# Optimization experiments

Hardware: AMD Instinct MI355X
Metric: run time of the kernel (lower is better)

The kernel has to match this reference:

```python
import jax, jax.numpy as jnp
import numpy as np

N, V, E, C_IN, C_OUT = 4, 4096, 2048, 64, 64


def setup_inputs() -> dict:
    key = jax.random.key(0)
    k_x, k_h, k_th = jax.random.split(key, 3)
    x = jax.random.normal(k_x, (N, V, C_IN), dtype=jnp.float32)
    H = (jax.random.uniform(k_h, (N, V, E)) < 0.05).astype(jnp.float32)
    # guarantee every vertex and every hyperedge has degree >= 1 (code divides by degree)
    v_idx = jnp.arange(V)
    H = H.at[:, v_idx, v_idx % E].set(1.0)
    # xavier_uniform for theta
    limit = float(np.sqrt(6.0 / (C_IN + C_OUT)))
    theta = jax.random.uniform(k_th, (C_IN, C_OUT), minval=-limit, maxval=limit, dtype=jnp.float32)
    bias = jnp.zeros((C_OUT,), dtype=jnp.float32)
    return {"x": x, "H": H, "theta": theta, "bias": bias}


def reference(x, H, theta, bias):
    # x: [N,V,C], H: [N,V,E] incidence, theta: [C,O], bias: [O]
    # Original builds diag_embed(1/deg) and multiplies; equivalent to direct
    # per-row / per-column scaling of H (same math, no NxVxV / NxExE diagonals).
    dv = 1.0 / H.sum(-1)            # [N,V] vertex degrees
    de = 1.0 / H.sum(1)             # [N,E] hyperedge degrees
    y = jnp.einsum('nvc,co->nvo', x, theta)          # [N,V,O]
    HDe = H * de[:, None, :]                          # H @ De  -> [N,V,E]
    y = jnp.einsum('nvc,nve->nec', y, HDe)            # vertex -> edge  [N,E,O]
    HDv = H * dv[:, :, None]                          # Dv @ H -> [N,V,E]
    y = jnp.einsum('nec,nve->nvc', y, HDv)            # edge -> vertex  [N,V,O]
    return y + bias[None, None, :]
```

## Files before the change

### kernel.cpp

```cpp
#include <hip/hip_runtime.h>
#include <hip/hip_bf16.h>
#include <stdint.h>

#define N_B 4
#define NV 4096
#define NE 2048
#define NC 64

typedef float    f32x4  __attribute__((ext_vector_type(4)));
typedef __bf16   bf16x8 __attribute__((ext_vector_type(8)));
typedef unsigned short u16;
typedef u16      u16x8  __attribute__((ext_vector_type(8)));
typedef uint32_t u32x4  __attribute__((ext_vector_type(4)));

__device__ __forceinline__ u16 f2bf_rne(float f) {
    uint32_t u = __builtin_bit_cast(uint32_t, f);
    u += 0x7FFFu + ((u >> 16) & 1u);
    return (u16)(u >> 16);
}
__device__ __forceinline__ float bf2f(u16 h) {
    uint32_t u = ((uint32_t)h) << 16;
    return __builtin_bit_cast(float, u);
}
__device__ __forceinline__ f32x4 mfma_bf16(u16x8 a, u16x8 b, f32x4 c) {
    return __builtin_amdgcn_mfma_f32_16x16x32_bf16(
        __builtin_bit_cast(bf16x8, a), __builtin_bit_cast(bf16x8, b), c, 0, 0, 0);
}
__device__ __forceinline__ u16x8 expand8(uint32_t byte) {
    u32x4 w;
#pragma unroll
    for (int p = 0; p < 4; ++p) {
        const uint32_t lo = (byte >> (2 * p)) & 1u;
        const uint32_t hi = (byte >> (2 * p + 1)) & 1u;
        w[p] = (lo | (hi << 16)) * 0x3F80u;
    }
    return __builtin_bit_cast(u16x8, w);
}

__global__ __launch_bounds__(256) void k_pack(const float* __restrict__ H,
                                              uint32_t* __restrict__ HB,
                                              uint32_t* __restrict__ HT,
                                              float* __restrict__ dvP,
                                              float* __restrict__ deP) {
    __shared__ float tile[64][65];
    const int n  = blockIdx.z;
    const int v0 = blockIdx.y * 64;
    const int e0 = blockIdx.x * 64;
    const int t = threadIdx.x, w = t >> 6, l = t & 63;

    const float* __restrict__ Hn = H + ((size_t)n * NV + v0) * NE + e0;

#pragma unroll 4
    for (int i = 0; i < 16; ++i) {
        const int row = w * 16 + i;
        const float h = Hn[(size_t)row * NE + l];
        tile[row][l] = h;
        const unsigned long long m = __ballot(h != 0.0f);
        if (l == 0)
            dvP[((size_t)blockIdx.x * N_B + n) * NV + v0 + row] = (float)__popcll(m);
        if (l < 2)
            HB[(((size_t)n * (NV / 16) + ((v0 + row) >> 4)) * (NE / 32) + (e0 >> 5) + l) * 16 +
               ((v0 + row) & 15)] = (uint32_t)(m >> (32 * l));
    }
    __syncthreads();

#pragma unroll 4
    for (int i = 0; i < 16; ++i) {
        const int col = w * 16 + i;
        const float h = tile[l][col];
        const unsigned long long m = __ballot(h != 0.0f);
        if (l == 0)
            deP[((size_t)blockIdx.y * N_B + n) * NE + e0 + col] = (float)__popcll(m);
        if (l < 2)
            HT[(((size_t)n * (NE / 16) + ((e0 + col) >> 4)) * (NV / 32) + (v0 >> 5) + l) * 16 +
               ((e0 + col) & 15)] = (uint32_t)(m >> (32 * l));
    }
}

__global__ __launch_bounds__(256) void k_deg(const float* __restrict__ dvP,
                                             const float* __restrict__ deP,
                                             float* __restrict__ dv,
                                             float* __restrict__ de) {
    const int id = blockIdx.x * 256 + threadIdx.x;
    if (id < N_B * NE) {
        float s = 0.f;
        for (int vt = 0; vt < 64; ++vt) s += deP[(size_t)vt * (N_B * NE) + id];
        de[id] = s;
    } else {
        const int j = id - N_B * NE;
        float s = 0.f;
        for (int et = 0; et < 32; ++et) s += dvP[(size_t)et * (N_B * NV) + j];
        dv[j] = s;
    }
}

__global__ __launch_bounds__(256) void k_xtheta(const float* __restrict__ x,
                                                const float* __restrict__ th,
                                                u16* __restrict__ Yh,
                                                u16* __restrict__ Yl) {
    __shared__ float xs[64][65];
    __shared__ float ts[64][65];
    const int t = threadIdx.x;
    const int n  = blockIdx.x >> 6;
    const int v0 = (blockIdx.x & 63) * 64;

#pragma unroll
    for (int i = 0; i < 4; ++i) {
        const int idx = i * 256 + t;
        const int row = idx >> 4, q = (idx & 15) * 4;
        const float4 xv = *(const float4*)&x[((size_t)(n * NV + v0 + row)) * 64 + q];
        const float4 tv = *(const float4*)&th[(size_t)row * 64 + q];
        xs[row][q] = xv.x; xs[row][q + 1] = xv.y; xs[row][q + 2] = xv.z; xs[row][q + 3] = xv.w;
        ts[row][q] = tv.x; ts[row][q + 1] = tv.y; ts[row][q + 2] = tv.z; ts[row][q + 3] = tv.w;
    }
    __syncthreads();

    const int v4 = (t & 15) * 4;
    const int c4 = (t >> 4) * 4;
    float acc[4][4] = {};
#pragma unroll
    for (int k = 0; k < 64; ++k) {
        float tv[4], xv[4];
#pragma unroll
        for (int i = 0; i < 4; ++i) { tv[i] = ts[k][c4 + i]; xv[i] = xs[v4 + i][k]; }
#pragma unroll
        for (int i = 0; i < 4; ++i)
#pragma unroll
            for (int j = 0; j < 4; ++j) acc[i][j] += tv[i] * xv[j];
    }
#pragma unroll
    for (int i = 0; i < 4; ++i) {
        ushort4 hi, lo;
        u16 h;
        h = f2bf_rne(acc[i][0]); hi.x = h; lo.x = f2bf_rne(acc[i][0] - bf2f(h));
        h = f2bf_rne(acc[i][1]); hi.y = h; lo.y = f2bf_rne(acc[i][1] - bf2f(h));
        h = f2bf_rne(acc[i][2]); hi.z = h; lo.z = f2bf_rne(acc[i][2] - bf2f(h));
        h = f2bf_rne(acc[i][3]); hi.w = h; lo.w = f2bf_rne(acc[i][3] - bf2f(h));
        const size_t o = ((size_t)n * 64 + c4 + i) * NV + v0 + v4;
        *(ushort4*)&Yh[o] = hi;
        *(ushort4*)&Yl[o] = lo;
    }
}

__global__ __launch_bounds__(256) void k_v2e(const uint32_t* __restrict__ HT,
                                             const u16* __restrict__ Yh,
                                             const u16* __restrict__ Yl,
                                             float* __restrict__ P2) {
    const int n  = blockIdx.z;
    const int sp = blockIdx.y;
    const int e0 = blockIdx.x * 64;
    const int krange = NV / gridDim.y;
    const int kk0 = sp * krange;
    const int S   = krange / 32;

    const int t = threadIdx.x, w = t >> 6, l = t & 63;
    const int lq = l >> 4, lr = l & 15;
    const int sh = lq * 8;

    const uint32_t* __restrict__ ht =
        HT + ((size_t)n * (NE / 16) + (e0 >> 4)) * ((NV / 32) * 16) + (kk0 >> 5) * 16 + lr;
    const u16* __restrict__ ybh = Yh + ((size_t)n * 64 + w * 16 + lr) * NV + kk0 + lq * 8;
    const u16* __restrict__ ybl = Yl + ((size_t)n * 64 + w * 16 + lr) * NV + kk0 + lq * 8;

    f32x4 acc0 = {0.f,0.f,0.f,0.f}, acc1 = acc0, acc2 = acc0, acc3 = acc0;

#pragma unroll 2
    for (int s = 0; s < S; ++s) {
        const u16x8 bh = *(const u16x8*)(ybh + s * 32);
        const u16x8 bl = *(const u16x8*)(ybl + s * 32);
        const uint32_t w0 = ht[0 * ((NV / 32) * 16) + s * 16];
        const uint32_t w1 = ht[1 * ((NV / 32) * 16) + s * 16];
        const uint32_t w2 = ht[2 * ((NV / 32) * 16) + s * 16];
        const uint32_t w3 = ht[3 * ((NV / 32) * 16) + s * 16];
        u16x8 a;
        a = expand8((w0 >> sh) & 0xFF);
        acc0 = mfma_bf16(a, bh, acc0); acc0 = mfma_bf16(a, bl, acc0);
        a = expand8((w1 >> sh) & 0xFF);
        acc1 = mfma_bf16(a, bh, acc1); acc1 = mfma_bf16(a, bl, acc1);
        a = expand8((w2 >> sh) & 0xFF);
        acc2 = mfma_bf16(a, bh, acc2); acc2 = mfma_bf16(a, bl, acc2);
        a = expand8((w3 >> sh) & 0xFF);
        acc3 = mfma_bf16(a, bh, acc3); acc3 = mfma_bf16(a, bl, acc3);
    }

    float* pb = P2 + (((size_t)sp * N_B + n) * 64 + w * 16 + lr) * NE + e0 + lq * 4;
    *(f32x4*)(pb + 0)  = acc0;
    *(f32x4*)(pb + 16) = acc1;
    *(f32x4*)(pb + 32) = acc2;
    *(f32x4*)(pb + 48) = acc3;
}

__global__ __launch_bounds__(256) void k_red2(const float* __restrict__ P2,
                                              const float* __restrict__ de,
                                              u16* __restrict__ Zh,
                                              u16* __restrict__ Zl, int nsp) {
    const int i = blockIdx.x * 256 + threadIdx.x;
    const int row = i >> 9;
    const int e4  = (i & 511) * 4;
    const int n   = row >> 6;

    float4 a = make_float4(0.f, 0.f, 0.f, 0.f);
    for (int sp = 0; sp < nsp; ++sp) {
        const float4 p = *(const float4*)&P2[((size_t)sp * 256 + row) * NE + e4];
        a.x += p.x; a.y += p.y; a.z += p.z; a.w += p.w;
    }
    const float4 d = *(const float4*)&de[(size_t)n * NE + e4];
    float z[4] = {a.x / d.x, a.y / d.y, a.z / d.z, a.w / d.w};
    ushort4 hi, lo;
    u16 h;
    h = f2bf_rne(z[0]); hi.x = h; lo.x = f2bf_rne(z[0] - bf2f(h));
    h = f2bf_rne(z[1]); hi.y = h; lo.y = f2bf_rne(z[1] - bf2f(h));
    h = f2bf_rne(z[2]); hi.z = h; lo.z = f2bf_rne(z[2] - bf2f(h));
    h = f2bf_rne(z[3]); hi.w = h; lo.w = f2bf_rne(z[3] - bf2f(h));
    *(ushort4*)&Zh[(size_t)row * NE + e4] = hi;
    *(ushort4*)&Zl[(size_t)row * NE + e4] = lo;
}

__global__ __launch_bounds__(256) void k_e2v(const uint32_t* __restrict__ HB,
                                             const u16* __restrict__ Zh,
                                             const u16* __restrict__ Zl,
                                             float* __restrict__ P3) {
    const int n  = blockIdx.z;
    const int sp = blockIdx.y;
    const int v0 = blockIdx.x * 64;
    const int krange = NE / gridDim.y;
    const int kk0 = sp * krange;
    const int S   = krange / 32;

    const int t = threadIdx.x, w = t >> 6, l = t & 63;
    const int lq = l >> 4, lr = l & 15;
    const int sh = lq * 8;

    const uint32_t* __restrict__ hb =
        HB + ((size_t)n * (NV / 16) + (v0 >> 4)) * ((NE / 32) * 16) + (kk0 >> 5) * 16 + lr;
    const u16* __restrict__ zbh = Zh + ((size_t)n * 64 + w * 16 + lr) * NE + kk0 + lq * 8;
    const u16* __restrict__ zbl = Zl + ((size_t)n * 64 + w * 16 + lr) * NE + kk0 + lq * 8;

    f32x4 acc0 = {0.f,0.f,0.f,0.f}, acc1 = acc0, acc2 = acc0, acc3 = acc0;

#pragma unroll 2
    for (int s = 0; s < S; ++s) {
        const u16x8 bh = *(const u16x8*)(zbh + s * 32);
        const u16x8 bl = *(const u16x8*)(zbl + s * 32);
        const uint32_t w0 = hb[0 * ((NE / 32) * 16) + s * 16];
        const uint32_t w1 = hb[1 * ((NE / 32) * 16) + s * 16];
        const uint32_t w2 = hb[2 * ((NE / 32) * 16) + s * 16];
        const uint32_t w3 = hb[3 * ((NE / 32) * 16) + s * 16];
        u16x8 a;
        a = expand8((w0 >> sh) & 0xFF);
        acc0 = mfma_bf16(a, bh, acc0); acc0 = mfma_bf16(a, bl, acc0);
        a = expand8((w1 >> sh) & 0xFF);
        acc1 = mfma_bf16(a, bh, acc1); acc1 = mfma_bf16(a, bl, acc1);
        a = expand8((w2 >> sh) & 0xFF);
        acc2 = mfma_bf16(a, bh, acc2); acc2 = mfma_bf16(a, bl, acc2);
        a = expand8((w3 >> sh) & 0xFF);
        acc3 = mfma_bf16(a, bh, acc3); acc3 = mfma_bf16(a, bl, acc3);
    }

    float* pb = P3 + (((size_t)sp * N_B + n) * 64 + w * 16 + lr) * NV + v0 + lq * 4;
    *(f32x4*)(pb + 0)  = acc0;
    *(f32x4*)(pb + 16) = acc1;
    *(f32x4*)(pb + 32) = acc2;
    *(f32x4*)(pb + 48) = acc3;
}

__global__ __launch_bounds__(512) void k_red3(const float* __restrict__ P3,
                                              const float* __restrict__ dv,
                                              const float* __restrict__ bias,
                                              float* __restrict__ out, int nsp) {
    __shared__ float lt[64][68];
    const int n  = blockIdx.y;
    const int v0 = blockIdx.x * 64;
    const int t  = threadIdx.x;

    {
        const int c   = t >> 3;
        const int vch = (t & 7) * 8;
        float4 s0 = make_float4(0.f, 0.f, 0.f, 0.f), s1 = s0;
        for (int sp = 0; sp < nsp; ++sp) {
            const size_t base = (((size_t)sp * N_B + n) * 64 + c) * NV + v0 + vch;
            const float4 p0 = *(const float4*)&P3[base];
            const float4 p1 = *(const float4*)&P3[base + 4];
            s0.x += p0.x; s0.y += p0.y; s0.z += p0.z; s0.w += p0.w;
            s1.x += p1.x; s1.y += p1.y; s1.z += p1.z; s1.w += p1.w;
        }
        *(float4*)&lt[c][vch]     = s0;
        *(float4*)&lt[c][vch + 4] = s1;
    }
    const int vw  = t >> 3;
    const int cch = (t & 7) * 8;
    const float dsum = dv[(size_t)n * NV + v0 + vw];
    __syncthreads();

    const float rdv = 1.0f / dsum;
    const float4 b0 = *(const float4*)&bias[cch];
    const float4 b1 = *(const float4*)&bias[cch + 4];
    float4 o0, o1;
    o0.x = lt[cch + 0][vw] * rdv + b0.x;
    o0.y = lt[cch + 1][vw] * rdv + b0.y;
    o0.z = lt[cch + 2][vw] * rdv + b0.z;
    o0.w = lt[cch + 3][vw] * rdv + b0.w;
    o1.x = lt[cch + 4][vw] * rdv + b1.x;
    o1.y = lt[cch + 5][vw] * rdv + b1.y;
    o1.z = lt[cch + 6][vw] * rdv + b1.z;
    o1.w = lt[cch + 7][vw] * rdv + b1.w;
    float* dst = out + ((size_t)n * NV + v0 + vw) * 64 + cch;
    *(float4*)dst       = o0;
    *(float4*)(dst + 4) = o1;
}

extern "C" void kernel_launch(void* const* d_in, const int* in_sizes, int n_in,
                              void* d_out, int out_size, void* d_ws, size_t ws_size,
                              hipStream_t stream) {
    const float* x     = (const float*)d_in[0];
    const float* H     = (const float*)d_in[1];
    const float* theta = (const float*)d_in[2];
    const float* bias  = (const float*)d_in[3];
    float* out = (float*)d_out;

    const size_t yE   = (size_t)N_B * 64 * NV;
    const size_t zE   = (size_t)N_B * 64 * NE;
    const size_t HBW  = (size_t)N_B * (NV / 16) * (NE / 32) * 16;
    const size_t HTW  = (size_t)N_B * (NE / 16) * (NV / 32) * 16;
    const size_t depE = (size_t)64 * N_B * NE;
    const size_t dvpE = (size_t)32 * N_B * NV;
    const size_t deE  = (size_t)N_B * NE;
    const size_t dvE  = (size_t)N_B * NV;

    u16* Yh = (u16*)d_ws;
    u16* Yl = Yh + yE;
    u16* Zh = Yl + yE;
    u16* Zl = Zh + zE;
    uint32_t* HB = (uint32_t*)(Zl + zE);
    uint32_t* HT = HB + HBW;
    float* deP = (float*)(HT + HTW);
    float* dvP = deP + depE;
    float* de  = dvP + dvpE;
    float* dv  = de + deE;
    float* fbase = dv + dvE;

    const size_t fixed_bytes = (size_t)((char*)fbase - (char*)d_ws);
    const size_t avail_f = (ws_size > fixed_bytes) ? (ws_size - fixed_bytes) / 4 : 0;

    const size_t unit2 = zE;
    const size_t unit3 = yE;
    int s2 = 1, s3 = 1;
    if      (avail_f >= 16 * unit2 + 8 * unit3) { s2 = 16; s3 = 8; }
    else if (avail_f >=  8 * unit2 + 4 * unit3) { s2 = 8;  s3 = 4; }
    else if (avail_f >=  4 * unit2 + 2 * unit3) { s2 = 4;  s3 = 2; }
    else if (avail_f >=  2 * unit2 + 1 * unit3) { s2 = 2;  s3 = 1; }

    float* P2 = fbase;
    float* P3 = P2 + (size_t)s2 * zE;

    k_pack<<<dim3(NE / 64, NV / 64, N_B), 256, 0, stream>>>(H, HB, HT, dvP, deP);
    k_xtheta<<<dim3(N_B * NV / 64), 256, 0, stream>>>(x, theta, Yh, Yl);
    k_deg<<<dim3((N_B * NE + N_B * NV) / 256), 256, 0, stream>>>(dvP, deP, dv, de);
    k_v2e<<<dim3(NE / 64, s2, N_B), 256, 0, stream>>>(HT, Yh, Yl, P2);
    k_red2<<<dim3((int)(zE / 4 / 256)), 256, 0, stream>>>(P2, de, Zh, Zl, s2);
    k_e2v<<<dim3(NV / 64, s3, N_B), 256, 0, stream>>>(HB, Zh, Zl, P3);
    k_red3<<<dim3(NV / 64, N_B), 512, 0, stream>>>(P3, dv, bias, out, s3);
}
```

Before: 120.2 us.

## Software-pipeline H and Y/Z loads in v2e/e2v kernels and halve split-K factor

Both sparse-dense MFMA kernels now prefetch the packed incidence words four steps ahead and double-buffer the bf16 hi/lo operand loads one step ahead, so global-load latency is hidden behind MFMA work. Launch bounds now request 4 blocks per SM to keep occupancy up despite the extra registers. The split-K factors drop from 16/8 to 8/4, which halves the partial-sum traffic the reduction kernels read but gives fewer blocks and longer loops per block. The main risks are register pressure from the prefetch buffers and lower parallelism from the smaller grid.

```diff
diff --git a/kernel.cpp b/kernel.cpp
--- a/kernel.cpp
+++ b/kernel.cpp
@@ -142,10 +142,10 @@
     }
 }
 
-__global__ __launch_bounds__(256) void k_v2e(const uint32_t* __restrict__ HT,
-                                             const u16* __restrict__ Yh,
-                                             const u16* __restrict__ Yl,
-                                             float* __restrict__ P2) {
+__global__ __launch_bounds__(256, 4) void k_v2e(const uint32_t* __restrict__ HT,
+                                                const u16* __restrict__ Yh,
+                                                const u16* __restrict__ Yl,
+                                                float* __restrict__ P2) {
     const int n  = blockIdx.z;
     const int sp = blockIdx.y;
     const int e0 = blockIdx.x * 64;
@@ -156,32 +156,64 @@
     const int t = threadIdx.x, w = t >> 6, l = t & 63;
     const int lq = l >> 4, lr = l & 15;
     const int sh = lq * 8;
+    const int hstride = (NV / 32) * 16;
 
     const uint32_t* __restrict__ ht =
-        HT + ((size_t)n * (NE / 16) + (e0 >> 4)) * ((NV / 32) * 16) + (kk0 >> 5) * 16 + lr;
+        HT + ((size_t)n * (NE / 16) + (e0 >> 4)) * hstride + (kk0 >> 5) * 16 + lr;
     const u16* __restrict__ ybh = Yh + ((size_t)n * 64 + w * 16 + lr) * NV + kk0 + lq * 8;
     const u16* __restrict__ ybl = Yl + ((size_t)n * 64 + w * 16 + lr) * NV + kk0 + lq * 8;
 
     f32x4 acc0 = {0.f,0.f,0.f,0.f}, acc1 = acc0, acc2 = acc0, acc3 = acc0;
 
-#pragma unroll 2
-    for (int s = 0; s < S; ++s) {
-        const u16x8 bh = *(const u16x8*)(ybh + s * 32);
-        const u16x8 bl = *(const u16x8*)(ybl + s * 32);
-        const uint32_t w0 = ht[0 * ((NV / 32) * 16) + s * 16];
-        const uint32_t w1 = ht[1 * ((NV / 32) * 16) + s * 16];
-        const uint32_t w2 = ht[2 * ((NV / 32) * 16) + s * 16];
-        const uint32_t w3 = ht[3 * ((NV / 32) * 16) + s * 16];
-        u16x8 a;
-        a = expand8((w0 >> sh) & 0xFF);
-        acc0 = mfma_bf16(a, bh, acc0); acc0 = mfma_bf16(a, bl, acc0);
-        a = expand8((w1 >> sh) & 0xFF);
-        acc1 = mfma_bf16(a, bh, acc1); acc1 = mfma_bf16(a, bl, acc1);
-        a = expand8((w2 >> sh) & 0xFF);
-        acc2 = mfma_bf16(a, bh, acc2); acc2 = mfma_bf16(a, bl, acc2);
-        a = expand8((w3 >> sh) & 0xFF);
-        acc3 = mfma_bf16(a, bh, acc3); acc3 = mfma_bf16(a, bl, acc3);
-    }
+    uint32_t A[4][4];
+#pragma unroll
+    for (int d = 0; d < 4; ++d) {
+        A[d][0] = ht[0 * hstride + d * 16];
+        A[d][1] = ht[1 * hstride + d * 16];
+        A[d][2] = ht[2 * hstride + d * 16];
+        A[d][3] = ht[3 * hstride + d * 16];
+    }
+    u16x8 BH[2], BL[2];
+    BH[0] = *(const u16x8*)ybh;
+    BL[0] = *(const u16x8*)ybl;
+
+#define V2E_STEP(s, u, GUARD_A, GUARD_B)                                      \
+    {                                                                         \
+        const uint32_t a0 = A[u][0], a1 = A[u][1], a2 = A[u][2], a3 = A[u][3];\
+        if (GUARD_A) {             \
+            A[u][0] = ht[0 * hstride + ((s) + 4) * 16];                       \
+            A[u][1] = ht[1 * hstride + ((s) + 4) * 16];                       \
+            A[u][2] = ht[2 * hstride + ((s) + 4) * 16];                       \
+            A[u][3] = ht[3 * hstride + ((s) + 4) * 16];                       \
+        }                                                                     \
+        if (GUARD_B) {                                                        \
+            BH[((u) + 1) & 1] = *(const u16x8*)(ybh + ((s) + 1) * 32);        \
+            BL[((u) + 1) & 1] = *(const u16x8*)(ybl + ((s) + 1) * 32);        \
+        }                                                                     \
+        const u16x8 bh = BH[(u) & 1], bl = BL[(u) & 1];                       \
+        u16x8 a;                                                              \
+        a = expand8((a0 >> sh) & 0xFF);                                       \
+        acc0 = mfma_bf16(a, bh, acc0); acc0 = mfma_bf16(a, bl, acc0);         \
+        a = expand8((a1 >> sh) & 0xFF);                                       \
+        acc1 = mfma_bf16(a, bh, acc1); acc1 = mfma_bf16(a, bl, acc1);         \
+        a = expand8((a2 >> sh) & 0xFF);                                       \
+        acc2 = mfma_bf16(a, bh, acc2); acc2 = mfma_bf16(a, bl, acc2);         \
+        a = expand8((a3 >> sh) & 0xFF);                                       \
+        acc3 = mfma_bf16(a, bh, acc3); acc3 = mfma_bf16(a, bl, acc3);         \
+    }
+
+    int sb = 0;
+    for (; sb < S - 4; sb += 4) {
+        V2E_STEP(sb + 0, 0, true, true)
+        V2E_STEP(sb + 1, 1, true, true)
+        V2E_STEP(sb + 2, 2, true, true)
+        V2E_STEP(sb + 3, 3, true, true)
+    }
+    V2E_STEP(sb + 0, 0, false, true)
+    V2E_STEP(sb + 1, 1, false, true)
+    V2E_STEP(sb + 2, 2, false, true)
+    V2E_STEP(sb + 3, 3, false, false)
+#undef V2E_STEP
 
     float* pb = P2 + (((size_t)sp * N_B + n) * 64 + w * 16 + lr) * NE + e0 + lq * 4;
     *(f32x4*)(pb + 0)  = acc0;
@@ -216,10 +248,10 @@
     *(ushort4*)&Zl[(size_t)row * NE + e4] = lo;
 }
 
-__global__ __launch_bounds__(256) void k_e2v(const uint32_t* __restrict__ HB,
-                                             const u16* __restrict__ Zh,
-                                             const u16* __restrict__ Zl,
-                                             float* __restrict__ P3) {
+__global__ __launch_bounds__(256, 4) void k_e2v(const uint32_t* __restrict__ HB,
+                                                const u16* __restrict__ Zh,
+                                                const u16* __restrict__ Zl,
+                                                float* __restrict__ P3) {
     const int n  = blockIdx.z;
     const int sp = blockIdx.y;
     const int v0 = blockIdx.x * 64;
@@ -230,32 +262,64 @@
     const int t = threadIdx.x, w = t >> 6, l = t & 63;
     const int lq = l >> 4, lr = l & 15;
     const int sh = lq * 8;
+    const int estride = (NE / 32) * 16;
 
     const uint32_t* __restrict__ hb =
-        HB + ((size_t)n * (NV / 16) + (v0 >> 4)) * ((NE / 32) * 16) + (kk0 >> 5) * 16 + lr;
+        HB + ((size_t)n * (NV / 16) + (v0 >> 4)) * estride + (kk0 >> 5) * 16 + lr;
     const u16* __restrict__ zbh = Zh + ((size_t)n * 64 + w * 16 + lr) * NE + kk0 + lq * 8;
     const u16* __restrict__ zbl = Zl + ((size_t)n * 64 + w * 16 + lr) * NE + kk0 + lq * 8;
 
     f32x4 acc0 = {0.f,0.f,0.f,0.f}, acc1 = acc0, acc2 = acc0, acc3 = acc0;
 
-#pragma unroll 2
-    for (int s = 0; s < S; ++s) {
-        const u16x8 bh = *(const u16x8*)(zbh + s * 32);
-        const u16x8 bl = *(const u16x8*)(zbl + s * 32);
-        const uint32_t w0 = hb[0 * ((NE / 32) * 16) + s * 16];
-        const uint32_t w1 = hb[1 * ((NE / 32) * 16) + s * 16];
-        const uint32_t w2 = hb[2 * ((NE / 32) * 16) + s * 16];
-        const uint32_t w3 = hb[3 * ((NE / 32) * 16) + s * 16];
-        u16x8 a;
-        a = expand8((w0 >> sh) & 0xFF);
-        acc0 = mfma_bf16(a, bh, acc0); acc0 = mfma_bf16(a, bl, acc0);
-        a = expand8((w1 >> sh) & 0xFF);
-        acc1 = mfma_bf16(a, bh, acc1); acc1 = mfma_bf16(a, bl, acc1);
-        a = expand8((w2 >> sh) & 0xFF);
-        acc2 = mfma_bf16(a, bh, acc2); acc2 = mfma_bf16(a, bl, acc2);
-        a = expand8((w3 >> sh) & 0xFF);
-        acc3 = mfma_bf16(a, bh, acc3); acc3 = mfma_bf16(a, bl, acc3);
-    }
+    uint32_t A[4][4];
+#pragma unroll
+    for (int d = 0; d < 4; ++d) {
+        A[d][0] = hb[0 * estride + d * 16];
+        A[d][1] = hb[1 * estride + d * 16];
+        A[d][2] = hb[2 * estride + d * 16];
+        A[d][3] = hb[3 * estride + d * 16];
+    }
+    u16x8 BH[2], BL[2];
+    BH[0] = *(const u16x8*)zbh;
+    BL[0] = *(const u16x8*)zbl;
+
+#define E2V_STEP(s, u, GUARD_A, GUARD_B)                                      \
+    {                                                                         \
+        const uint32_t a0 = A[u][0], a1 = A[u][1], a2 = A[u][2], a3 = A[u][3];\
+        if (GUARD_A) {                                                        \
+            A[u][0] = hb[0 * estride + ((s) + 4) * 16];                       \
+            A[u][1] = hb[1 * estride + ((s) + 4) * 16];                       \
+            A[u][2] = hb[2 * estride + ((s) + 4) * 16];                       \
+            A[u][3] = hb[3 * estride + ((s) + 4) * 16];                       \
+        }                                                                     \
+        if (GUARD_B) {                                                        \
+            BH[((u) + 1) & 1] = *(const u16x8*)(zbh + ((s) + 1) * 32);        \
+            BL[((u) + 1) & 1] = *(const u16x8*)(zbl + ((s) + 1) * 32);        \
+        }                                                                     \
+        const u16x8 bh = BH[(u) & 1], bl = BL[(u) & 1];                       \
+        u16x8 a;                                                              \
+        a = expand8((a0 >> sh) & 0xFF);                                       \
+        acc0 = mfma_bf16(a, bh, acc0); acc0 = mfma_bf16(a, bl, acc0);         \
+        a = expand8((a1 >> sh) & 0xFF);                                       \
+        acc1 = mfma_bf16(a, bh, acc1); acc1 = mfma_bf16(a, bl, acc1);         \
+        a = expand8((a2 >> sh) & 0xFF);                                       \
+        acc2 = mfma_bf16(a, bh, acc2); acc2 = mfma_bf16(a, bl, acc2);         \
+        a = expand8((a3 >> sh) & 0xFF);                                       \
+        acc3 = mfma_bf16(a, bh, acc3); acc3 = mfma_bf16(a, bl, acc3);         \
+    }
+
+    int sb = 0;
+    for (; sb < S - 4; sb += 4) {
+        E2V_STEP(sb + 0, 0, true, true)
+        E2V_STEP(sb + 1, 1, true, true)
+        E2V_STEP(sb + 2, 2, true, true)
+        E2V_STEP(sb + 3, 3, true, true)
+    }
+    E2V_STEP(sb + 0, 0, false, true)
+    E2V_STEP(sb + 1, 1, false, true)
+    E2V_STEP(sb + 2, 2, false, true)
+    E2V_STEP(sb + 3, 3, false, false)
+#undef E2V_STEP
 
     float* pb = P3 + (((size_t)sp * N_B + n) * 64 + w * 16 + lr) * NV + v0 + lq * 4;
     *(f32x4*)(pb + 0)  = acc0;
@@ -345,10 +409,9 @@
     const size_t unit2 = zE;
     const size_t unit3 = yE;
     int s2 = 1, s3 = 1;
-    if      (avail_f >= 16 * unit2 + 8 * unit3) { s2 = 16; s3 = 8; }
-    else if (avail_f >=  8 * unit2 + 4 * unit3) { s2 = 8;  s3 = 4; }
-    else if (avail_f >=  4 * unit2 + 2 * unit3) { s2 = 4;  s3 = 2; }
-    else if (avail_f >=  2 * unit2 + 1 * unit3) { s2 = 2;  s3 = 1; }
+    if      (avail_f >= 8 * unit2 + 4 * unit3) { s2 = 8; s3 = 4; }
+    else if (avail_f >= 4 * unit2 + 2 * unit3) { s2 = 4; s3 = 2; }
+    else if (avail_f >= 2 * unit2 + 1 * unit3) { s2 = 2; s3 = 1; }
 
     float* P2 = fbase;
     float* P3 = P2 + (size_t)s2 * zE;
```

Result: faster. 106.4 us (-11.5%).
